# Kernel tuning notes

Hardware: AMD Instinct MI355X
Metric: run time of the kernel (lower is better)

Reference implementation:

```python
import jax, jax.numpy as jnp
import numpy as np

N, C, CI, H, W = 4, 512, 256, 64, 64  # batch, in_channels, inter_channels, spatial
EPS = 1e-5


def conv1x1(x, w, b):
    # x: (N,C,H,W), w: (O,C), b: (O,)
    return jnp.einsum('nchw,oc->nohw', x, w) + b[None, :, None, None]


def setup_inputs() -> dict:
    key = jax.random.key(0)
    ks = jax.random.split(key, 11)
    s = 0.02
    return {
        'x': jax.random.normal(ks[0], (N, C, H, W), dtype=jnp.float32),
        'g_w': jax.random.normal(ks[1], (CI, C), dtype=jnp.float32) * s,
        'g_b': jax.random.normal(ks[2], (CI,), dtype=jnp.float32) * s,
        'theta_w': jax.random.normal(ks[3], (CI, C), dtype=jnp.float32) * s,
        'theta_b': jax.random.normal(ks[4], (CI,), dtype=jnp.float32) * s,
        'phi_w': jax.random.normal(ks[5], (CI, C), dtype=jnp.float32) * s,
        'phi_b': jax.random.normal(ks[6], (CI,), dtype=jnp.float32) * s,
        'wz_w': jax.random.normal(ks[7], (C, CI), dtype=jnp.float32) * s,
        'wz_b': jax.random.normal(ks[8], (C,), dtype=jnp.float32) * s,
        'bn_gamma': jax.random.normal(ks[9], (C,), dtype=jnp.float32) * 0.1 + 1.0,
        'bn_beta': jax.random.normal(ks[10], (C,), dtype=jnp.float32) * 0.1,
    }


def reference(x, g_w, g_b, theta_w, theta_b, phi_w, phi_b, wz_w, wz_b, bn_gamma, bn_beta):
    # NLBlockND.forward_self, mode='embedded', dimension=2, bn_layer=True
    n = x.shape[0]
    L = x.shape[2] * x.shape[3]  # H*W tokens
    g_x = conv1x1(x, g_w, g_b).reshape(n, CI, L)          # (N,Ci,L)
    theta_x = conv1x1(x, theta_w, theta_b).reshape(n, CI, L)
    phi_x = conv1x1(x, phi_w, phi_b).reshape(n, CI, L)
    f = jnp.einsum('ncl,ncm->nlm', theta_x, phi_x)        # (N,L,L) = theta^T @ phi
    f_div_C = jax.nn.softmax(f, axis=-1)
    y = jnp.einsum('nlm,ncm->ncl', f_div_C, g_x)          # (N,Ci,L) = (attn @ g)^T
    y = y.reshape(n, CI, x.shape[2], x.shape[3])
    w_y = conv1x1(y, wz_w, wz_b)                          # (N,C,H,W)
    # BatchNorm2d, training-mode batch statistics (biased variance)
    mean = jnp.mean(w_y, axis=(0, 2, 3), keepdims=True)
    var = jnp.var(w_y, axis=(0, 2, 3), keepdims=True)
    w_y = (w_y - mean) * jax.lax.rsqrt(var + EPS)
    w_y = w_y * bn_gamma[None, :, None, None] + bn_beta[None, :, None, None]
    return w_y + x
```

## Files before the change

### kernel.cpp

```cpp
#include <hip/hip_runtime.h>
#include <hip/hip_bf16.h>


#define NB    4
#define CDIM  512
#define CIDIM 256
#define LDIM  4096
#define BN_EPS 1e-5f

typedef unsigned short u16;
typedef __attribute__((ext_vector_type(8))) short short8;
typedef __attribute__((ext_vector_type(4))) float f32x4;
typedef __attribute__((ext_vector_type(4))) unsigned short u16x4;

#define WY_OFF    0
#define THPH_OFF  8388608
#define G_OFF     12582912
#define Y_OFF     14680064
#define WTS_OFF   16777216
#define BIAS2_OFF 17039360
#define ML_OFF    17039872
#define ST_OFF    17105408

__device__ __forceinline__ u16 f2b(float f) {
    union { float f; unsigned u; } v; v.f = f;
    return (u16)((v.u + 0x7FFFu + ((v.u >> 16) & 1u)) >> 16);
}

__device__ __forceinline__ void gl_lds16(const u16* g, u16* l) {
    __builtin_amdgcn_global_load_lds(
        (const __attribute__((address_space(1))) void*)g,
        (__attribute__((address_space(3))) void*)l, 16, 0, 0);
}

__global__ void transpose_x(const float* __restrict__ x, u16* __restrict__ xt) {
    __shared__ float tile[32][33];
    int n = blockIdx.z;
    int l0 = blockIdx.x * 32, c0 = blockIdx.y * 32;
    const float* xn = x + (size_t)n * CDIM * LDIM;
    u16* xtn = xt + (size_t)n * LDIM * CDIM;
    int tx = threadIdx.x, ty = threadIdx.y;
#pragma unroll
    for (int k = 0; k < 4; k++)
        tile[ty + 8 * k][tx] = xn[(size_t)(c0 + ty + 8 * k) * LDIM + l0 + tx];
    __syncthreads();
#pragma unroll
    for (int k = 0; k < 4; k++)
        xtn[(size_t)(l0 + ty + 8 * k) * CDIM + c0 + tx] = f2b(tile[tx][ty + 8 * k]);
}

__global__ void cast_w(const float* __restrict__ gw, const float* __restrict__ tw,
                       const float* __restrict__ pw, const float* __restrict__ zw,
                       u16* __restrict__ out) {
    int idx = blockIdx.x * 256 + threadIdx.x;
    if (idx >= 4 * 131072) return;
    int seg = idx >> 17, off = idx & 131071;
    const float* s = (seg == 0) ? gw : (seg == 1) ? tw : (seg == 2) ? pw : zw;
    out[idx] = f2b(s[off]);
}

__global__ void concat_bias(const float* __restrict__ tb, const float* __restrict__ pb,
                            float* __restrict__ out) {
    int i = blockIdx.x * 256 + threadIdx.x;
    if (i < 256) out[i] = tb[i];
    else if (i < 512) out[i] = pb[i - 256];
}

template <int BIAS_MODE, bool OUT_BF16>
__global__ __launch_bounds__(256)
void gemm_nt(const u16* __restrict__ A, const u16* __restrict__ B,
             void* __restrict__ Dv, const float* __restrict__ bias,
             int K, int lda, int ldb, int ldd,
             long batchA, long batchB, long batchD) {
    __shared__ __align__(16) u16 As[128 * 32];
    __shared__ __align__(16) u16 Bs[128 * 32];
    int z = blockIdx.z;
    A += (size_t)z * batchA;
    B += (size_t)z * batchB;

    int tid = threadIdx.x, lane = tid & 63, wave = tid >> 6;
    int n0 = blockIdx.x * 128, m0 = blockIdx.y * 128;
    int wr = wave >> 1, wc = wave & 1;

    f32x4 acc[4][4];
#pragma unroll
    for (int i = 0; i < 4; i++)
#pragma unroll
        for (int j = 0; j < 4; j++) acc[i][j] = (f32x4){0.f, 0.f, 0.f, 0.f};

    int sr = wave * 16 + (lane >> 2);
    int ss = ((lane & 3) ^ ((lane >> 2) & 3)) * 8;
    const u16* Ag0 = A + (size_t)(m0 + sr) * lda + ss;
    const u16* Ag1 = A + (size_t)(m0 + 64 + sr) * lda + ss;
    const u16* Bg0 = B + (size_t)(n0 + sr) * ldb + ss;
    const u16* Bg1 = B + (size_t)(n0 + 64 + sr) * ldb + ss;
    u16* Al0 = &As[(wave * 16) * 32];
    u16* Al1 = &As[(64 + wave * 16) * 32];
    u16* Bl0 = &Bs[(wave * 16) * 32];
    u16* Bl1 = &Bs[(64 + wave * 16) * 32];

    int koff = ((lane >> 4) ^ (lane & 3)) * 8;
    int ra = (wr * 64 + (lane & 15)) * 32 + koff;
    int rb = (wc * 64 + (lane & 15)) * 32 + koff;

    for (int k0 = 0; k0 < K; k0 += 32) {
        __syncthreads();
        gl_lds16(Ag0 + k0, Al0);
        gl_lds16(Ag1 + k0, Al1);
        gl_lds16(Bg0 + k0, Bl0);
        gl_lds16(Bg1 + k0, Bl1);
        __syncthreads();

        short8 af[4], bf[4];
#pragma unroll
        for (int mt = 0; mt < 4; mt++) af[mt] = *(const short8*)&As[ra + mt * 16 * 32];
#pragma unroll
        for (int nt = 0; nt < 4; nt++) bf[nt] = *(const short8*)&Bs[rb + nt * 16 * 32];
#pragma unroll
        for (int mt = 0; mt < 4; mt++)
#pragma unroll
            for (int nt = 0; nt < 4; nt++)
                acc[mt][nt] = __builtin_amdgcn_mfma_f32_16x16x32_bf16(
                    af[mt], bf[nt], acc[mt][nt], 0, 0, 0);
    }

#pragma unroll
    for (int mt = 0; mt < 4; mt++) {
        int mg = m0 + wr * 64 + mt * 16 + (lane >> 4) * 4;
#pragma unroll
        for (int nt = 0; nt < 4; nt++) {
            int ng = n0 + wc * 64 + nt * 16 + (lane & 15);
#pragma unroll
            for (int r = 0; r < 4; r++) {
                float v = acc[mt][nt][r];
                if (BIAS_MODE == 1) v += bias[mg + r];
                if (BIAS_MODE == 2) v += bias[ng];
                if (OUT_BF16) {
                    u16* D = (u16*)Dv + (size_t)z * batchD;
                    D[(size_t)(mg + r) * ldd + ng] = f2b(v);
                } else {
                    float* D = (float*)Dv + (size_t)z * batchD;
                    D[(size_t)(mg + r) * ldd + ng] = v;
                }
            }
        }
    }
}

__global__ __launch_bounds__(256)
void flash_attn(const u16* __restrict__ THPH, const u16* __restrict__ G,
                float* __restrict__ OP, float* __restrict__ ML) {
    __shared__ __align__(16) u16 Ks[64 * 256];
    __shared__ __align__(16) u16 Vs[256 * 64];
    __shared__ __align__(16) u16 Ps[4][16][72];

    int b = blockIdx.x;
    int n = b & 3;
    int m = b >> 2;
    int qt = m >> 1;
    int jh = m & 1;
    int q0 = qt * 64;

    const u16* TH = THPH + (size_t)n * LDIM * 512;
    const u16* PH = TH + 256;
    const u16* Gn = G + (size_t)n * LDIM * CIDIM;
    float* OPh = OP + ((size_t)jh * NB + n) * LDIM * CIDIM;
    float* MLh = ML + ((size_t)jh * NB + n) * LDIM * 2;

    int tid = threadIdx.x, lane = tid & 63, wave = tid >> 6;
    int quad = lane >> 4, lan = lane & 15;

    short8 qf[8];
    {
        const u16* qb = TH + (size_t)(q0 + wave * 16 + lan) * 512 + quad * 8;
#pragma unroll
        for (int kf = 0; kf < 8; kf++) qf[kf] = *(const short8*)(qb + kf * 32);
    }

    int krow0 = wave * 16 + (lane >> 5);
    int vrow0 = wave * 64 + (lane >> 3);
    int vslot = ((lane & 7) ^ ((lane >> 3) & 7)) * 8;

    f32x4 o[16];
#pragma unroll
    for (int i = 0; i < 16; i++) o[i] = (f32x4){0.f, 0.f, 0.f, 0.f};
    float mrow[4] = {-1e30f, -1e30f, -1e30f, -1e30f};
    float lrow[4] = {0.f, 0.f, 0.f, 0.f};

#pragma unroll 1
    for (int jt = 0; jt < 32; jt++) {
        int j0 = (jh * 32 + jt) * 64;
        __syncthreads();
#pragma unroll
        for (int i = 0; i < 8; i++) {
            int r = krow0 + 2 * i;
            int s = ((lane & 31) ^ (r & 7)) * 8;
            gl_lds16(PH + (size_t)(j0 + r) * 512 + s,
                     &Ks[(wave * 16 + 2 * i) * 256]);
        }
#pragma unroll
        for (int i = 0; i < 8; i++) {
            int r = vrow0 + 8 * i;
            gl_lds16(Gn + (size_t)r * LDIM + j0 + vslot,
                     &Vs[(wave * 64 + 8 * i) * 64]);
        }
        __syncthreads();

        f32x4 s[4];
#pragma unroll
        for (int ct = 0; ct < 4; ct++) s[ct] = (f32x4){0.f, 0.f, 0.f, 0.f};
#pragma unroll
        for (int kf = 0; kf < 8; kf++)
#pragma unroll
            for (int ct = 0; ct < 4; ct++) {
                int row = ct * 16 + lan;
                short8 bb = *(const short8*)&Ks[row * 256 +
                                (((kf * 4 + quad) ^ (lan & 7)) << 3)];
                s[ct] = __builtin_amdgcn_mfma_f32_16x16x32_bf16(qf[kf], bb, s[ct], 0, 0, 0);
            }

        float alpha[4];
#pragma unroll
        for (int r = 0; r < 4; r++) {
            float mx = fmaxf(fmaxf(s[0][r], s[1][r]), fmaxf(s[2][r], s[3][r]));
#pragma unroll
            for (int msk = 1; msk <= 8; msk <<= 1)
                mx = fmaxf(mx, __shfl_xor(mx, msk, 64));
            float mnew = fmaxf(mrow[r], mx);
            alpha[r] = __expf(mrow[r] - mnew);
            float rs = 0.f;
#pragma unroll
            for (int ct = 0; ct < 4; ct++) {
                float p = __expf(s[ct][r] - mnew);
                rs += p;
                Ps[wave][quad * 4 + r][ct * 16 + lan] = f2b(p);
            }
#pragma unroll
            for (int msk = 1; msk <= 8; msk <<= 1)
                rs += __shfl_xor(rs, msk, 64);
            lrow[r] = lrow[r] * alpha[r] + rs;
            mrow[r] = mnew;
        }
#pragma unroll
        for (int ot = 0; ot < 16; ot++)
#pragma unroll
            for (int r = 0; r < 4; r++) o[ot][r] *= alpha[r];

#pragma unroll
        for (int kf2 = 0; kf2 < 2; kf2++) {
            short8 a = *(const short8*)&Ps[wave][lan][kf2 * 32 + quad * 8];
#pragma unroll
            for (int ot = 0; ot < 16; ot++) {
                int row = ot * 16 + lan;
                short8 bb = *(const short8*)&Vs[row * 64 +
                                (((kf2 * 4 + quad) ^ (lan & 7)) << 3)];
                o[ot] = __builtin_amdgcn_mfma_f32_16x16x32_bf16(a, bb, o[ot], 0, 0, 0);
            }
        }
    }

#pragma unroll
    for (int r = 0; r < 4; r++) {
        int row = q0 + wave * 16 + quad * 4 + r;
        if (lan == 0) {
            MLh[row * 2] = mrow[r];
            MLh[row * 2 + 1] = lrow[r];
        }
#pragma unroll
        for (int ot = 0; ot < 16; ot++)
            OPh[(size_t)row * CIDIM + ot * 16 + lan] = o[ot][r];
    }
}

__global__ void merge_y(const float* __restrict__ OP, const float* __restrict__ ML,
                        u16* __restrict__ Y) {
    const size_t HALF = (size_t)NB * LDIM * CIDIM;
    const int HALF_ML = NB * LDIM * 2;
    int i4 = blockIdx.x * 256 + threadIdx.x;
    int row = i4 >> 6;
    float ma = ML[row * 2], la = ML[row * 2 + 1];
    float mb = ML[HALF_ML + row * 2], lb = ML[HALF_ML + row * 2 + 1];
    float M = fmaxf(ma, mb);
    float ea = __expf(ma - M), eb = __expf(mb - M);
    float inv = 1.f / (la * ea + lb * eb);
    float4 oa = ((const float4*)OP)[i4];
    float4 ob = ((const float4*)(OP + HALF))[i4];
    u16x4 y;
    y.x = f2b((oa.x * ea + ob.x * eb) * inv);
    y.y = f2b((oa.y * ea + ob.y * eb) * inv);
    y.z = f2b((oa.z * ea + ob.z * eb) * inv);
    y.w = f2b((oa.w * ea + ob.w * eb) * inv);
    ((u16x4*)Y)[i4] = y;
}

__global__ void bn_stats_kernel(const float* __restrict__ WY, float* __restrict__ stats) {
    int o = blockIdx.x, tid = threadIdx.x, lane = tid & 63, wave = tid >> 6;
    float s = 0.f, s2 = 0.f;
    for (int n = 0; n < NB; n++) {
        const float4* p = (const float4*)(WY + (size_t)(n * CDIM + o) * LDIM);
        for (int i = tid; i < LDIM / 4; i += 256) {
            float4 v = p[i];
            s += v.x + v.y + v.z + v.w;
            s2 += v.x * v.x + v.y * v.y + v.z * v.z + v.w * v.w;
        }
    }
    for (int o2 = 32; o2 > 0; o2 >>= 1) {
        s += __shfl_xor(s, o2, 64);
        s2 += __shfl_xor(s2, o2, 64);
    }
    __shared__ float rs[4], rs2[4];
    if (lane == 0) { rs[wave] = s; rs2[wave] = s2; }
    __syncthreads();
    if (tid == 0) {
        float S = rs[0] + rs[1] + rs[2] + rs[3];
        float S2 = rs2[0] + rs2[1] + rs2[2] + rs2[3];
        const float cnt = (float)(NB * LDIM);
        float mean = S / cnt;
        float var = S2 / cnt - mean * mean;
        stats[o] = mean;
        stats[CDIM + o] = rsqrtf(var + BN_EPS);
    }
}

__global__ void bn_apply_kernel(const float* __restrict__ WY, const float* __restrict__ stats,
                                const float* __restrict__ x,
                                const float* __restrict__ gamma, const float* __restrict__ beta,
                                float* __restrict__ out) {
    int i4 = blockIdx.x * 256 + threadIdx.x;
    int o = (i4 >> 10) & (CDIM - 1);
    float m = stats[o], is = stats[CDIM + o];
    float ga = gamma[o], be = beta[o];
    float4 w = ((const float4*)WY)[i4];
    float4 xv = ((const float4*)x)[i4];
    float4 r;
    r.x = (w.x - m) * is * ga + be + xv.x;
    r.y = (w.y - m) * is * ga + be + xv.y;
    r.z = (w.z - m) * is * ga + be + xv.z;
    r.w = (w.w - m) * is * ga + be + xv.w;
    ((float4*)out)[i4] = r;
}

extern "C" void kernel_launch(void* const* d_in, const int* in_sizes, int n_in,
                              void* d_out, int out_size, void* d_ws, size_t ws_size,
                              hipStream_t stream) {
    const float* x   = (const float*)d_in[0];
    const float* gw  = (const float*)d_in[1];
    const float* gb  = (const float*)d_in[2];
    const float* tw  = (const float*)d_in[3];
    const float* tb  = (const float*)d_in[4];
    const float* pw  = (const float*)d_in[5];
    const float* pb  = (const float*)d_in[6];
    const float* zw  = (const float*)d_in[7];
    const float* zb  = (const float*)d_in[8];
    const float* bng = (const float*)d_in[9];
    const float* bnb = (const float*)d_in[10];
    float* out = (float*)d_out;
    float* ws  = (float*)d_ws;

    float* WY   = ws + WY_OFF;
    u16*   xT   = (u16*)(ws + WY_OFF);
    float* OP   = ws + WY_OFF;
    u16*   THPH = (u16*)(ws + THPH_OFF);
    u16*   G    = (u16*)(ws + G_OFF);
    u16*   Y    = (u16*)(ws + Y_OFF);
    u16*   WB   = (u16*)(ws + WTS_OFF);
    float* BC   = ws + BIAS2_OFF;
    float* ML   = ws + ML_OFF;
    float* ST   = ws + ST_OFF;

    const long LC   = (long)LDIM * CDIM;
    const long LCI  = (long)LDIM * CIDIM;
    const long L512 = (long)LDIM * 512;
    const long CL   = (long)CDIM * LDIM;

    transpose_x<<<dim3(LDIM / 32, CDIM / 32, NB), dim3(32, 8), 0, stream>>>(x, xT);
    cast_w<<<2048, 256, 0, stream>>>(gw, tw, pw, zw, WB);
    concat_bias<<<2, 256, 0, stream>>>(tb, pb, BC);

    gemm_nt<2, true><<<dim3(4, 32, NB), 256, 0, stream>>>(
        xT, WB + 131072, THPH, BC, CDIM, CDIM, CDIM, 512, LC, 0, L512);
    gemm_nt<1, true><<<dim3(32, 2, NB), 256, 0, stream>>>(
        WB, xT, G, gb, CDIM, CDIM, CDIM, LDIM, 0, LC, LCI);

    flash_attn<<<dim3(512), 256, 0, stream>>>(THPH, G, OP, ML);
    merge_y<<<dim3(NB * LDIM * CIDIM / 4 / 256), 256, 0, stream>>>(OP, ML, Y);

    gemm_nt<1, false><<<dim3(32, 4, NB), 256, 0, stream>>>(
        WB + 393216, Y, (void*)WY, zb, CIDIM, CIDIM, CIDIM, LDIM, 0, LCI, CL);

    bn_stats_kernel<<<dim3(CDIM), 256, 0, stream>>>(WY, ST);
    bn_apply_kernel<<<dim3(NB * CDIM * LDIM / 4 / 256), 256, 0, stream>>>(
        WY, ST, x, bng, bnb, out);
}
```

Baseline: 319.8 us.

## Rework flash attention with 32x32 MFMA, register-held P, 4-way KV split

The attention kernel switches from 16x16x32 to 32x32x16 MFMA tiles with 128-query blocks and transposed S (K as A operand). The probabilities now stay in registers and are exchanged across half-waves with shuffles instead of going through LDS. The KV range is split four ways instead of two. Partial outputs are stored as bf16 in channel-major layout, and the max/sum statistics are packed as fp16 pairs. The merge kernel now combines four partials and transposes through LDS. This cuts LDS traffic and partial-output bandwidth, at some cost in precision from the fp16 max/sum and bf16 partials, and with more register pressure.

New measurement: 328.7 us. +2.8%, slower.

```diff
diff --git a/kernel.cpp b/kernel.cpp
--- a/kernel.cpp
+++ b/kernel.cpp
@@ -1,5 +1,6 @@
 #include <hip/hip_runtime.h>
 #include <hip/hip_bf16.h>
+#include <hip/hip_fp16.h>
 
 
 #define NB    4
@@ -11,7 +12,7 @@
 typedef unsigned short u16;
 typedef __attribute__((ext_vector_type(8))) short short8;
 typedef __attribute__((ext_vector_type(4))) float f32x4;
-typedef __attribute__((ext_vector_type(4))) unsigned short u16x4;
+typedef __attribute__((ext_vector_type(16))) float f32x16;
 
 #define WY_OFF    0
 #define THPH_OFF  8388608
@@ -25,6 +26,14 @@
 __device__ __forceinline__ u16 f2b(float f) {
     union { float f; unsigned u; } v; v.f = f;
     return (u16)((v.u + 0x7FFFu + ((v.u >> 16) & 1u)) >> 16);
+}
+
+__device__ __forceinline__ float b2f(u16 x) {
+    return __uint_as_float((unsigned)x << 16);
+}
+
+__device__ __forceinline__ unsigned pack2(float a, float b) {
+    return (unsigned)f2b(a) | ((unsigned)f2b(b) << 16);
 }
 
 __device__ __forceinline__ void gl_lds16(const u16* g, u16* l) {
@@ -147,150 +156,199 @@
     }
 }
 
-__global__ __launch_bounds__(256)
+__global__ __launch_bounds__(256, 2)
 void flash_attn(const u16* __restrict__ THPH, const u16* __restrict__ G,
-                float* __restrict__ OP, float* __restrict__ ML) {
+                u16* __restrict__ OPB, unsigned* __restrict__ ML4) {
     __shared__ __align__(16) u16 Ks[64 * 256];
     __shared__ __align__(16) u16 Vs[256 * 64];
-    __shared__ __align__(16) u16 Ps[4][16][72];
 
     int b = blockIdx.x;
     int n = b & 3;
-    int m = b >> 2;
-    int qt = m >> 1;
-    int jh = m & 1;
-    int q0 = qt * 64;
+    int jh = (b >> 2) & 3;
+    int qt = b >> 4;
+    int q0 = qt * 128;
 
     const u16* TH = THPH + (size_t)n * LDIM * 512;
     const u16* PH = TH + 256;
     const u16* Gn = G + (size_t)n * LDIM * CIDIM;
-    float* OPh = OP + ((size_t)jh * NB + n) * LDIM * CIDIM;
-    float* MLh = ML + ((size_t)jh * NB + n) * LDIM * 2;
-
-    int tid = threadIdx.x, lane = tid & 63, wave = tid >> 6;
-    int quad = lane >> 4, lan = lane & 15;
-
-    short8 qf[8];
+    u16* OPh = OPB + ((size_t)jh * NB + n) * CIDIM * LDIM;
+    unsigned* MLh = ML4 + ((size_t)jh * NB + n) * LDIM;
+
+    int tid = threadIdx.x, lane = tid & 63, w = tid >> 6;
+    int h = lane >> 5, lq = lane & 31, l7 = lane & 7;
+
+    short8 qf[16];
     {
-        const u16* qb = TH + (size_t)(q0 + wave * 16 + lan) * 512 + quad * 8;
-#pragma unroll
-        for (int kf = 0; kf < 8; kf++) qf[kf] = *(const short8*)(qb + kf * 32);
-    }
-
-    int krow0 = wave * 16 + (lane >> 5);
-    int vrow0 = wave * 64 + (lane >> 3);
-    int vslot = ((lane & 7) ^ ((lane >> 3) & 7)) * 8;
-
-    f32x4 o[16];
-#pragma unroll
-    for (int i = 0; i < 16; i++) o[i] = (f32x4){0.f, 0.f, 0.f, 0.f};
-    float mrow[4] = {-1e30f, -1e30f, -1e30f, -1e30f};
-    float lrow[4] = {0.f, 0.f, 0.f, 0.f};
+        const u16* qb = TH + (size_t)(q0 + w * 32 + lq) * 512 + h * 8;
+#pragma unroll
+        for (int c = 0; c < 16; c++) qf[c] = *(const short8*)(qb + c * 16);
+    }
+
+    f32x16 o[8];
+#pragma unroll
+    for (int i = 0; i < 8; i++)
+#pragma unroll
+        for (int e = 0; e < 16; e++) o[i][e] = 0.f;
+    float m = -3e38f, lsum = 0.f;
+
+    int krh = lane >> 5;
+    int ksl = lane & 31;
+    int vr = lane >> 3;
+    int vsl = (lane & 7) ^ vr;
+
+#define STAGE(jt_) do {                                                        \
+    int j0_ = (jh * 16 + (jt_)) * 64;                                          \
+    _Pragma("unroll")                                                          \
+    for (int i = 0; i < 8; i++) {                                              \
+        int r = w * 16 + 2 * i + krh;                                          \
+        int s = ksl ^ (r & 7);                                                 \
+        gl_lds16(PH + (size_t)(j0_ + r) * 512 + s * 8,                         \
+                 &Ks[(w * 16 + 2 * i) * 256]);                                 \
+    }                                                                          \
+    _Pragma("unroll")                                                          \
+    for (int i = 0; i < 8; i++) {                                              \
+        int r = w * 64 + 8 * i + vr;                                           \
+        gl_lds16(Gn + (size_t)r * LDIM + j0_ + vsl * 8,                        \
+                 &Vs[(w * 64 + 8 * i) * 64]);                                  \
+    }                                                                          \
+} while (0)
 
 #pragma unroll 1
-    for (int jt = 0; jt < 32; jt++) {
-        int j0 = (jh * 32 + jt) * 64;
+    for (int jt = 0; jt < 16; jt++) {
         __syncthreads();
-#pragma unroll
-        for (int i = 0; i < 8; i++) {
-            int r = krow0 + 2 * i;
-            int s = ((lane & 31) ^ (r & 7)) * 8;
-            gl_lds16(PH + (size_t)(j0 + r) * 512 + s,
-                     &Ks[(wave * 16 + 2 * i) * 256]);
+        STAGE(jt);
+        __syncthreads();
+
+        f32x16 sv[2];
+#pragma unroll
+        for (int t = 0; t < 2; t++) {
+            f32x16 a;
+#pragma unroll
+            for (int e = 0; e < 16; e++) a[e] = 0.f;
+#pragma unroll
+            for (int c = 0; c < 16; c++) {
+                int slot = (c * 2 + h) ^ l7;
+                short8 ka = *(const short8*)&Ks[(t * 32 + lq) * 256 + slot * 8];
+                a = __builtin_amdgcn_mfma_f32_32x32x16_bf16(ka, qf[c], a, 0, 0, 0);
+            }
+            sv[t] = a;
         }
-#pragma unroll
-        for (int i = 0; i < 8; i++) {
-            int r = vrow0 + 8 * i;
-            gl_lds16(Gn + (size_t)r * LDIM + j0 + vslot,
-                     &Vs[(wave * 64 + 8 * i) * 64]);
-        }
-        __syncthreads();
-
-        f32x4 s[4];
-#pragma unroll
-        for (int ct = 0; ct < 4; ct++) s[ct] = (f32x4){0.f, 0.f, 0.f, 0.f};
-#pragma unroll
-        for (int kf = 0; kf < 8; kf++)
-#pragma unroll
-            for (int ct = 0; ct < 4; ct++) {
-                int row = ct * 16 + lan;
-                short8 bb = *(const short8*)&Ks[row * 256 +
-                                (((kf * 4 + quad) ^ (lan & 7)) << 3)];
-                s[ct] = __builtin_amdgcn_mfma_f32_16x16x32_bf16(qf[kf], bb, s[ct], 0, 0, 0);
+
+        float tm = sv[0][0];
+#pragma unroll
+        for (int r = 1; r < 16; r++) tm = fmaxf(tm, sv[0][r]);
+#pragma unroll
+        for (int r = 0; r < 16; r++) tm = fmaxf(tm, sv[1][r]);
+        tm = fmaxf(tm, __shfl_xor(tm, 32, 64));
+
+        float mnew = fmaxf(m, tm);
+        float al = __expf(m - mnew);
+        m = mnew;
+        lsum *= al;
+#pragma unroll
+        for (int i = 0; i < 8; i++)
+#pragma unroll
+            for (int e = 0; e < 16; e++) o[i][e] *= al;
+
+        float rs = 0.f;
+#pragma unroll
+        for (int t = 0; t < 2; t++)
+#pragma unroll
+            for (int r = 0; r < 16; r++) {
+                float p = __expf(sv[t][r] - m);
+                sv[t][r] = p;
+                rs += p;
             }
-
-        float alpha[4];
-#pragma unroll
-        for (int r = 0; r < 4; r++) {
-            float mx = fmaxf(fmaxf(s[0][r], s[1][r]), fmaxf(s[2][r], s[3][r]));
-#pragma unroll
-            for (int msk = 1; msk <= 8; msk <<= 1)
-                mx = fmaxf(mx, __shfl_xor(mx, msk, 64));
-            float mnew = fmaxf(mrow[r], mx);
-            alpha[r] = __expf(mrow[r] - mnew);
-            float rs = 0.f;
-#pragma unroll
-            for (int ct = 0; ct < 4; ct++) {
-                float p = __expf(s[ct][r] - mnew);
-                rs += p;
-                Ps[wave][quad * 4 + r][ct * 16 + lan] = f2b(p);
-            }
-#pragma unroll
-            for (int msk = 1; msk <= 8; msk <<= 1)
-                rs += __shfl_xor(rs, msk, 64);
-            lrow[r] = lrow[r] * alpha[r] + rs;
-            mrow[r] = mnew;
-        }
-#pragma unroll
-        for (int ot = 0; ot < 16; ot++)
-#pragma unroll
-            for (int r = 0; r < 4; r++) o[ot][r] *= alpha[r];
-
-#pragma unroll
-        for (int kf2 = 0; kf2 < 2; kf2++) {
-            short8 a = *(const short8*)&Ps[wave][lan][kf2 * 32 + quad * 8];
-#pragma unroll
-            for (int ot = 0; ot < 16; ot++) {
-                int row = ot * 16 + lan;
-                short8 bb = *(const short8*)&Vs[row * 64 +
-                                (((kf2 * 4 + quad) ^ (lan & 7)) << 3)];
-                o[ot] = __builtin_amdgcn_mfma_f32_16x16x32_bf16(a, bb, o[ot], 0, 0, 0);
+        lsum += rs + __shfl_xor(rs, 32, 64);
+
+#pragma unroll
+        for (int t = 0; t < 2; t++) {
+#pragma unroll
+            for (int s2 = 0; s2 < 2; s2++) {
+                int st = t * 2 + s2;
+                int r0 = 8 * s2;
+                float e0 = sv[t][r0 + 0], e1 = sv[t][r0 + 1];
+                float e2 = sv[t][r0 + 2], e3 = sv[t][r0 + 3];
+                float e4 = sv[t][r0 + 4], e5 = sv[t][r0 + 5];
+                float e6 = sv[t][r0 + 6], e7 = sv[t][r0 + 7];
+                unsigned own_a = h ? pack2(e4, e5) : pack2(e0, e1);
+                unsigned own_b = h ? pack2(e6, e7) : pack2(e2, e3);
+                unsigned snd_a = h ? pack2(e0, e1) : pack2(e4, e5);
+                unsigned snd_b = h ? pack2(e2, e3) : pack2(e6, e7);
+                unsigned rcv_a = __shfl_xor(snd_a, 32, 64);
+                unsigned rcv_b = __shfl_xor(snd_b, 32, 64);
+                union { unsigned u[4]; short8 v; } pf;
+                pf.u[0] = h ? rcv_a : own_a;
+                pf.u[1] = h ? rcv_b : own_b;
+                pf.u[2] = h ? own_a : rcv_a;
+                pf.u[3] = h ? own_b : rcv_b;
+                int slot = (st * 2 + h) ^ l7;
+#pragma unroll
+                for (int cit = 0; cit < 8; cit++) {
+                    short8 va = *(const short8*)&Vs[(cit * 32 + lq) * 64 + slot * 8];
+                    o[cit] = __builtin_amdgcn_mfma_f32_32x32x16_bf16(va, pf.v, o[cit], 0, 0, 0);
+                }
             }
         }
     }
 
-#pragma unroll
-    for (int r = 0; r < 4; r++) {
-        int row = q0 + wave * 16 + quad * 4 + r;
-        if (lan == 0) {
-            MLh[row * 2] = mrow[r];
-            MLh[row * 2 + 1] = lrow[r];
+    int q = q0 + w * 32 + lq;
+    if (h == 0) {
+        unsigned pm = (unsigned)__half_as_ushort(__float2half(m));
+        unsigned pl = (unsigned)__half_as_ushort(__float2half(lsum));
+        MLh[q] = pm | (pl << 16);
+    }
+#pragma unroll
+    for (int cit = 0; cit < 8; cit++)
+#pragma unroll
+        for (int rr = 0; rr < 16; rr++) {
+            int ci = cit * 32 + (rr & 3) + 8 * (rr >> 2) + 4 * h;
+            OPh[(size_t)ci * LDIM + q] = f2b(o[cit][rr]);
         }
-#pragma unroll
-        for (int ot = 0; ot < 16; ot++)
-            OPh[(size_t)row * CIDIM + ot * 16 + lan] = o[ot][r];
-    }
-}
-
-__global__ void merge_y(const float* __restrict__ OP, const float* __restrict__ ML,
+#undef STAGE
+}
+
+__global__ void merge_y(const u16* __restrict__ OPB, const unsigned* __restrict__ ML4,
                         u16* __restrict__ Y) {
-    const size_t HALF = (size_t)NB * LDIM * CIDIM;
-    const int HALF_ML = NB * LDIM * 2;
-    int i4 = blockIdx.x * 256 + threadIdx.x;
-    int row = i4 >> 6;
-    float ma = ML[row * 2], la = ML[row * 2 + 1];
-    float mb = ML[HALF_ML + row * 2], lb = ML[HALF_ML + row * 2 + 1];
-    float M = fmaxf(ma, mb);
-    float ea = __expf(ma - M), eb = __expf(mb - M);
-    float inv = 1.f / (la * ea + lb * eb);
-    float4 oa = ((const float4*)OP)[i4];
-    float4 ob = ((const float4*)(OP + HALF))[i4];
-    u16x4 y;
-    y.x = f2b((oa.x * ea + ob.x * eb) * inv);
-    y.y = f2b((oa.y * ea + ob.y * eb) * inv);
-    y.z = f2b((oa.z * ea + ob.z * eb) * inv);
-    y.w = f2b((oa.w * ea + ob.w * eb) * inv);
-    ((u16x4*)Y)[i4] = y;
+    __shared__ u16 tile[32][33];
+    int nn = blockIdx.z;
+    int l0 = blockIdx.x * 32, ci0 = blockIdx.y * 32;
+    int tx = threadIdx.x, ty = threadIdx.y;
+    int l = l0 + tx;
+
+    float mq[4], lq[4];
+#pragma unroll
+    for (int q = 0; q < 4; q++) {
+        unsigned u = ML4[((size_t)q * NB + nn) * LDIM + l];
+        mq[q] = __half2float(__ushort_as_half((unsigned short)(u & 0xffff)));
+        lq[q] = __half2float(__ushort_as_half((unsigned short)(u >> 16)));
+    }
+    float M = fmaxf(fmaxf(mq[0], mq[1]), fmaxf(mq[2], mq[3]));
+    float wq[4];
+    float den = 0.f;
+#pragma unroll
+    for (int q = 0; q < 4; q++) {
+        wq[q] = __expf(mq[q] - M);
+        den += lq[q] * wq[q];
+    }
+    float inv = 1.f / den;
+#pragma unroll
+    for (int q = 0; q < 4; q++) wq[q] *= inv;
+
+#pragma unroll
+    for (int k = 0; k < 4; k++) {
+        int ci = ci0 + ty + 8 * k;
+        float acc = 0.f;
+#pragma unroll
+        for (int q = 0; q < 4; q++)
+            acc += b2f(OPB[((size_t)q * NB + nn) * CIDIM * LDIM + (size_t)ci * LDIM + l]) * wq[q];
+        tile[ty + 8 * k][tx] = f2b(acc);
+    }
+    __syncthreads();
+    u16* Yn = Y + (size_t)nn * LDIM * CIDIM;
+#pragma unroll
+    for (int k = 0; k < 4; k++)
+        Yn[(size_t)(l0 + ty + 8 * k) * CIDIM + ci0 + tx] = tile[tx][ty + 8 * k];
 }
 
 __global__ void bn_stats_kernel(const float* __restrict__ WY, float* __restrict__ stats) {
@@ -357,16 +415,16 @@
     float* out = (float*)d_out;
     float* ws  = (float*)d_ws;
 
-    float* WY   = ws + WY_OFF;
-    u16*   xT   = (u16*)(ws + WY_OFF);
-    float* OP   = ws + WY_OFF;
-    u16*   THPH = (u16*)(ws + THPH_OFF);
-    u16*   G    = (u16*)(ws + G_OFF);
-    u16*   Y    = (u16*)(ws + Y_OFF);
-    u16*   WB   = (u16*)(ws + WTS_OFF);
-    float* BC   = ws + BIAS2_OFF;
-    float* ML   = ws + ML_OFF;
-    float* ST   = ws + ST_OFF;
+    float*    WY   = ws + WY_OFF;
+    u16*      xT   = (u16*)(ws + WY_OFF);
+    u16*      OPB  = (u16*)(ws + WY_OFF);
+    u16*      THPH = (u16*)(ws + THPH_OFF);
+    u16*      G    = (u16*)(ws + G_OFF);
+    u16*      Y    = (u16*)(ws + Y_OFF);
+    u16*      WB   = (u16*)(ws + WTS_OFF);
+    float*    BC   = ws + BIAS2_OFF;
+    unsigned* ML4  = (unsigned*)(ws + ML_OFF);
+    float*    ST   = ws + ST_OFF;
 
     const long LC   = (long)LDIM * CDIM;
     const long LCI  = (long)LDIM * CIDIM;
@@ -382,8 +440,8 @@
     gemm_nt<1, true><<<dim3(32, 2, NB), 256, 0, stream>>>(
         WB, xT, G, gb, CDIM, CDIM, CDIM, LDIM, 0, LC, LCI);
 
-    flash_attn<<<dim3(512), 256, 0, stream>>>(THPH, G, OP, ML);
-    merge_y<<<dim3(NB * LDIM * CIDIM / 4 / 256), 256, 0, stream>>>(OP, ML, Y);
+    flash_attn<<<dim3(512), 256, 0, stream>>>(THPH, G, OPB, ML4);
+    merge_y<<<dim3(LDIM / 32, CIDIM / 32, NB), dim3(32, 8), 0, stream>>>(OPB, ML4, Y);
 
     gemm_nt<1, false><<<dim3(32, 4, NB), 256, 0, stream>>>(
         WB + 393216, Y, (void*)WY, zb, CIDIM, CIDIM, CIDIM, LDIM, 0, LCI, CL);
```
